# Optimization experiments

Measured on AMD Instinct MI355X. Metric: run time of the kernel, lower is better.

The kernel has to match this reference:

```python
import jax, jax.numpy as jnp
import numpy as np

B, IN, N, OUT = 65536, 512, 256, 64  # batch, in_size, neurons, out_size


def setup_inputs() -> dict:
    key = jax.random.key(0)
    k1, k2, k3, k4 = jax.random.split(key, 4)
    return {
        "x": jax.random.normal(k1, (B, IN), jnp.float32),
        "W_lin": jax.random.normal(k2, (IN, N + OUT), jnp.float32),   # nlinear
        "W_nl": jax.random.normal(k3, (N - 1, N), jnp.float32),        # padded nonlinear[i] rows
        "W_out": jax.random.normal(k4, (OUT, N), jnp.float32),         # output_weights[0:out_size]
    }


def reference(x, W_lin, W_nl, W_out):
    act = jnp.tanh
    lin = x @ W_lin  # [B, N+OUT]
    # row i of nonlinear weights is valid only for entries 0..i (length i+1)
    tri_mask = (jnp.arange(N)[None, :] <= jnp.arange(N - 1)[:, None]).astype(lin.dtype)
    Wm = W_nl * tri_mask  # [N-1, N]
    # growing accumulator, fixed-size buffer; position 0 = lin[0] + 1
    acc0 = jnp.zeros((x.shape[0], N), lin.dtype).at[:, 0].set(lin[:, 0] + 1.0)
    col = jnp.arange(N)[None, :]

    def step(acc, inp):
        w, l, i = inp  # w: [N] masked weights, l: [B] = lin[:, i], i: scalar step
        v = jnp.sum(act(acc) * w[None, :], axis=1) + l + 1.0  # [B]
        acc = jnp.where(col == (i + 1), v[:, None], acc)
        return acc, None

    xs = (Wm, lin[:, : N - 1].T, jnp.arange(N - 1))
    acc, _ = jax.lax.scan(step, acc0, xs)
    # outs[i] = act(t) @ output_weights[i] + lin[neurons + i] + 1
    out = act(acc) @ W_out.T + lin[:, N:] + 1.0  # [B, OUT]
    return out
```

## Files before the change

### kernel.cpp

```cpp
#include <hip/hip_runtime.h>
#include <hip/hip_bf16.h>

typedef _Float16 f16x8 __attribute__((ext_vector_type(8)));
typedef unsigned short u16x8 __attribute__((ext_vector_type(8)));
typedef float f32x4 __attribute__((ext_vector_type(4)));
typedef unsigned int u32x4 __attribute__((ext_vector_type(4)));

static __device__ __forceinline__ unsigned short h2u(_Float16 h) {
    return __builtin_bit_cast(unsigned short, h);
}
static __device__ __forceinline__ float fast_tanh(float x) {
    float e = __expf(2.0f * x);
    return 1.0f - 2.0f / (e + 1.0f);
}

__global__ void cascade_prep(const float* __restrict__ W_lin,
                             const float* __restrict__ W_nl,
                             const float* __restrict__ W_out,
                             unsigned short* __restrict__ wlin_h,
                             unsigned short* __restrict__ wlin_l,
                             unsigned short* __restrict__ wnl_h,
                             unsigned short* __restrict__ wnl_l,
                             unsigned short* __restrict__ wout_h,
                             unsigned short* __restrict__ wout_l,
                             float* __restrict__ wcol) {
    int idx = blockIdx.x * blockDim.x + threadIdx.x;
    int stride = gridDim.x * blockDim.x;
    for (int i = idx; i < 320 * 512; i += stride) {
        int n = i >> 9, k = i & 511;
        float w = W_lin[k * 320 + n];
        _Float16 h = (_Float16)w;
        wlin_h[i] = h2u(h);
        wlin_l[i] = h2u((_Float16)(w - (float)h));
    }
    for (int i = idx; i < 255 * 256; i += stride) {
        int r = i >> 8, k = i & 255;
        float w = (k <= r) ? W_nl[i] : 0.0f;
        _Float16 h = (_Float16)w;
        wnl_h[i] = h2u(h);
        wnl_l[i] = h2u((_Float16)(w - (float)h));
    }
    for (int i = idx; i < 64 * 256; i += stride) {
        float w = W_out[i];
        _Float16 h = (_Float16)w;
        wout_h[i] = h2u(h);
        wout_l[i] = h2u((_Float16)(w - (float)h));
    }
    for (int i = idx; i < 256; i += stride) {
        int b = i >> 5, u = i & 31;
        float* dst = wcol + b * 496 + (31 * u - (u * (u - 1)) / 2);
        for (int j = u + 1; j < 32; ++j)
            dst[j - u - 1] = W_nl[(size_t)(b * 32 + j - 1) * 256 + b * 32 + u];
    }
}

__global__ __launch_bounds__(512, 1) void lin_gemm(
    const float* __restrict__ x,
    const unsigned short* __restrict__ wlin_h,
    const unsigned short* __restrict__ wlin_l,
    float* __restrict__ linc,
    float* __restrict__ lino) {

    __shared__ _Float16 bufH[2][16 * 520];
    __shared__ _Float16 bufL[2][16 * 520];

    const int tid = threadIdx.x;
    const int wv  = tid >> 6;
    const int l15 = tid & 15;
    const int g   = (tid & 63) >> 4;
    const long row0 = (long)blockIdx.x * 128;

    f16x8 xfh[16], xfl[16];
    {
        const float* xp = x + (row0 + wv * 16 + l15) * 512 + g * 8;
        #pragma unroll
        for (int ks = 0; ks < 16; ++ks) {
            float4 p0 = *reinterpret_cast<const float4*>(xp + ks * 32);
            float4 p1 = *reinterpret_cast<const float4*>(xp + ks * 32 + 4);
            float av[8] = {p0.x, p0.y, p0.z, p0.w, p1.x, p1.y, p1.z, p1.w};
            f16x8 fh, fl;
            #pragma unroll
            for (int e = 0; e < 8; ++e) {
                _Float16 hh = (_Float16)av[e];
                fh[e] = hh;
                fl[e] = (_Float16)(av[e] - (float)hh);
            }
            xfh[ks] = fh;
            xfl[ks] = fl;
        }
    }

    u16x8 rh[2], rl[2];
    #define STAGE_LOAD(nt)                                                     \
        {                                                                      \
            _Pragma("unroll")                                                  \
            for (int it = 0; it < 2; ++it) {                                   \
                int flat = it * 4096 + tid * 8;                                \
                int r = flat >> 9, c = flat & 511;                             \
                rh[it] = *reinterpret_cast<const u16x8*>(                      \
                    wlin_h + (size_t)((nt) * 16 + r) * 512 + c);               \
                rl[it] = *reinterpret_cast<const u16x8*>(                      \
                    wlin_l + (size_t)((nt) * 16 + r) * 512 + c);               \
            }                                                                  \
        }
    #define STAGE_WRITE(buf)                                                   \
        {                                                                      \
            _Pragma("unroll")                                                  \
            for (int it = 0; it < 2; ++it) {                                   \
                int flat = it * 4096 + tid * 8;                                \
                int r = flat >> 9, c = flat & 511;                             \
                *reinterpret_cast<u16x8*>(&bufH[buf][r * 520 + c]) =           \
                    __builtin_bit_cast(u16x8, rh[it]);                         \
                *reinterpret_cast<u16x8*>(&bufL[buf][r * 520 + c]) =           \
                    __builtin_bit_cast(u16x8, rl[it]);                         \
            }                                                                  \
        }

    STAGE_LOAD(0);
    STAGE_WRITE(0);
    __syncthreads();

    int cur = 0;
    for (int nt = 0; nt < 20; ++nt) {
        if (nt < 19) STAGE_LOAD(nt + 1);

        f32x4 acc = (f32x4){0.f, 0.f, 0.f, 0.f};
        if (nt < 16) {
            #pragma unroll
            for (int ks = 0; ks < 16; ++ks) {
                f16x8 bh = *reinterpret_cast<const f16x8*>(
                    &bufH[cur][l15 * 520 + ks * 32 + g * 8]);
                f16x8 bl = *reinterpret_cast<const f16x8*>(
                    &bufL[cur][l15 * 520 + ks * 32 + g * 8]);
                acc = __builtin_amdgcn_mfma_f32_16x16x32_f16(xfh[ks], bh, acc, 0, 0, 0);
                acc = __builtin_amdgcn_mfma_f32_16x16x32_f16(xfl[ks], bh, acc, 0, 0, 0);
                acc = __builtin_amdgcn_mfma_f32_16x16x32_f16(xfh[ks], bl, acc, 0, 0, 0);
            }
            #pragma unroll
            for (int j = 0; j < 4; ++j)
                linc[(row0 + wv * 16 + g * 4 + j) * 256 + nt * 16 + l15] = acc[j];
        } else {
            #pragma unroll
            for (int ks = 0; ks < 16; ++ks) {
                f16x8 bh = *reinterpret_cast<const f16x8*>(
                    &bufH[cur][l15 * 520 + ks * 32 + g * 8]);
                acc = __builtin_amdgcn_mfma_f32_16x16x32_f16(xfh[ks], bh, acc, 0, 0, 0);
            }
            #pragma unroll
            for (int j = 0; j < 4; ++j)
                lino[(row0 + wv * 16 + g * 4 + j) * 64 + (nt - 16) * 16 + l15] = acc[j];
        }

        if (nt < 19) STAGE_WRITE(cur ^ 1);
        __syncthreads();
        cur ^= 1;
    }
    #undef STAGE_LOAD
    #undef STAGE_WRITE
}

static __device__ __forceinline__ void hist_frag(const unsigned int* hp,
                                                 f16x8* ah, f16x8* al) {
    u32x4 a0 = *reinterpret_cast<const u32x4*>(hp);
    u32x4 a1 = *reinterpret_cast<const u32x4*>(hp + 4);
    u32x4 hx, lx;
    hx[0] = (a0[0] & 0xffffu) | (a0[1] << 16);
    hx[1] = (a0[2] & 0xffffu) | (a0[3] << 16);
    hx[2] = (a1[0] & 0xffffu) | (a1[1] << 16);
    hx[3] = (a1[2] & 0xffffu) | (a1[3] << 16);
    lx[0] = (a0[0] >> 16) | (a0[1] & 0xffff0000u);
    lx[1] = (a0[2] >> 16) | (a0[3] & 0xffff0000u);
    lx[2] = (a1[0] >> 16) | (a1[1] & 0xffff0000u);
    lx[3] = (a1[2] >> 16) | (a1[3] & 0xffff0000u);
    *ah = __builtin_bit_cast(f16x8, hx);
    *al = __builtin_bit_cast(f16x8, lx);
}

__global__ __launch_bounds__(64, 2) void cascade_casc(
    float* linc,
    const float* __restrict__ lino,
    const float* __restrict__ wcol,
    const unsigned short* __restrict__ wnl_h,
    const unsigned short* __restrict__ wnl_l,
    const unsigned short* __restrict__ wout_h,
    const unsigned short* __restrict__ wout_l,
    float* __restrict__ out) {

    __shared__ float conT[32 * 36];
    __shared__ float linT[32 * 36];
    __shared__ float wslab[500];

    const int l   = threadIdx.x;
    const int l15 = l & 15;
    const int g   = l >> 4;
    const int r   = l & 31;
    const long row0 = (long)blockIdx.x * 32;

    unsigned int* histc = reinterpret_cast<unsigned int*>(linc);
    float carry = 0.0f;

    for (int b = 0; b < 8; ++b) {
        #pragma unroll
        for (int it = 0; it < 4; ++it) {
            int flat = it * 256 + l * 4;
            int rr = flat >> 5, c4 = flat & 31;
            float4 v = *reinterpret_cast<const float4*>(
                linc + (row0 + rr) * 256 + b * 32 + c4);
            *reinterpret_cast<float4*>(&linT[rr * 36 + c4]) = v;
        }
        {
            int i0 = l * 4;
            if (i0 < 496) {
                float4 v = *reinterpret_cast<const float4*>(wcol + b * 496 + i0);
                *reinterpret_cast<float4*>(&wslab[i0]) = v;
            }
            int i1 = 256 + l * 4;
            if (i1 < 496) {
                float4 v = *reinterpret_cast<const float4*>(wcol + b * 496 + i1);
                *reinterpret_cast<float4*>(&wslab[i1]) = v;
            }
        }

        f32x4 accC[2][2];
        #pragma unroll
        for (int m = 0; m < 2; ++m)
            #pragma unroll
            for (int n2 = 0; n2 < 2; ++n2)
                accC[m][n2] = (f32x4){0.f, 0.f, 0.f, 0.f};
        for (int kc = 0; kc < b; ++kc) {
            f16x8 ah[2], al[2];
            #pragma unroll
            for (int m = 0; m < 2; ++m)
                hist_frag(histc + (row0 + m * 16 + l15) * 256 + kc * 32 + g * 8,
                          &ah[m], &al[m]);
            #pragma unroll
            for (int n2 = 0; n2 < 2; ++n2) {
                const size_t wrow = (size_t)(b * 32 + n2 * 16 + l15 - 1) * 256 + kc * 32 + g * 8;
                f16x8 bh = __builtin_bit_cast(f16x8, *reinterpret_cast<const u16x8*>(wnl_h + wrow));
                f16x8 bl = __builtin_bit_cast(f16x8, *reinterpret_cast<const u16x8*>(wnl_l + wrow));
                #pragma unroll
                for (int m = 0; m < 2; ++m) {
                    accC[m][n2] = __builtin_amdgcn_mfma_f32_16x16x32_f16(ah[m], bh, accC[m][n2], 0, 0, 0);
                    accC[m][n2] = __builtin_amdgcn_mfma_f32_16x16x32_f16(al[m], bh, accC[m][n2], 0, 0, 0);
                    accC[m][n2] = __builtin_amdgcn_mfma_f32_16x16x32_f16(ah[m], bl, accC[m][n2], 0, 0, 0);
                }
            }
        }
        #pragma unroll
        for (int m = 0; m < 2; ++m)
            #pragma unroll
            for (int n2 = 0; n2 < 2; ++n2)
                #pragma unroll
                for (int j = 0; j < 4; ++j)
                    conT[(m * 16 + g * 4 + j) * 36 + n2 * 16 + l15] = accC[m][n2][j];
        __syncthreads();

        if (b == 0) carry = linT[r * 36];

        float acc[32];
        #pragma unroll
        for (int j = 0; j < 32; ++j) acc[j] = 0.0f;
        float lastlin = carry;
        #pragma unroll
        for (int u8 = 0; u8 < 4; ++u8) {
            float4 cw0 = *reinterpret_cast<const float4*>(&conT[r * 36 + u8 * 8]);
            float4 cw1 = *reinterpret_cast<const float4*>(&conT[r * 36 + u8 * 8 + 4]);
            float4 lw0 = *reinterpret_cast<const float4*>(&linT[r * 36 + u8 * 8]);
            float4 lw1 = *reinterpret_cast<const float4*>(&linT[r * 36 + u8 * 8 + 4]);
            float conw[8] = {cw0.x, cw0.y, cw0.z, cw0.w, cw1.x, cw1.y, cw1.z, cw1.w};
            float linw[8] = {lw0.x, lw0.y, lw0.z, lw0.w, lw1.x, lw1.y, lw1.z, lw1.w};
            unsigned int pk[8];
            #pragma unroll
            for (int v = 0; v < 8; ++v) {
                const int u = u8 * 8 + v;
                float lv = (v == 0) ? lastlin : linw[v - 1];
                float vv = acc[u] + conw[v] + lv + 1.0f;
                float tv = fast_tanh(vv);
                _Float16 hv = (_Float16)tv;
                _Float16 lo = (_Float16)(tv - (float)hv);
                pk[v] = (unsigned int)h2u(hv) | ((unsigned int)h2u(lo) << 16);
                const float* wu = wslab + (31 * u - (u * (u - 1)) / 2);
                #pragma unroll
                for (int j = u + 1; j < 32; ++j)
                    acc[j] = fmaf(tv, wu[j - u - 1], acc[j]);
            }
            lastlin = linw[7];
            if (l < 32) {
                long hb = (row0 + r) * 256 + b * 32 + u8 * 8;
                *reinterpret_cast<u32x4*>(histc + hb) = (u32x4){pk[0], pk[1], pk[2], pk[3]};
                *reinterpret_cast<u32x4*>(histc + hb + 4) = (u32x4){pk[4], pk[5], pk[6], pk[7]};
            }
        }
        carry = lastlin;
        __syncthreads();
    }

    #pragma unroll
    for (int m = 0; m < 2; ++m) {
        #pragma unroll
        for (int n = 0; n < 4; ++n) {
            f32x4 acc = (f32x4){0.f, 0.f, 0.f, 0.f};
            #pragma unroll
            for (int kc = 0; kc < 8; ++kc) {
                f16x8 ah, al;
                hist_frag(histc + (row0 + m * 16 + l15) * 256 + kc * 32 + g * 8, &ah, &al);
                const size_t wrow = (size_t)(n * 16 + l15) * 256 + kc * 32 + g * 8;
                f16x8 bh = __builtin_bit_cast(f16x8, *reinterpret_cast<const u16x8*>(wout_h + wrow));
                f16x8 bl = __builtin_bit_cast(f16x8, *reinterpret_cast<const u16x8*>(wout_l + wrow));
                acc = __builtin_amdgcn_mfma_f32_16x16x32_f16(ah, bh, acc, 0, 0, 0);
                acc = __builtin_amdgcn_mfma_f32_16x16x32_f16(al, bh, acc, 0, 0, 0);
                acc = __builtin_amdgcn_mfma_f32_16x16x32_f16(ah, bl, acc, 0, 0, 0);
            }
            #pragma unroll
            for (int j = 0; j < 4; ++j) {
                long rr = row0 + m * 16 + g * 4 + j;
                int c = n * 16 + l15;
                out[rr * 64 + c] = acc[j] + lino[rr * 64 + c] + 1.0f;
            }
        }
    }
}

extern "C" void kernel_launch(void* const* d_in, const int* in_sizes, int n_in,
                              void* d_out, int out_size, void* d_ws, size_t ws_size,
                              hipStream_t stream) {
    (void)in_sizes; (void)n_in; (void)out_size; (void)ws_size;
    const float* x     = (const float*)d_in[0];
    const float* W_lin = (const float*)d_in[1];
    const float* W_nl  = (const float*)d_in[2];
    const float* W_out = (const float*)d_in[3];
    float* out = (float*)d_out;

    char* ws = (char*)d_ws;
    unsigned short* wlin_h = (unsigned short*)(ws);
    unsigned short* wlin_l = (unsigned short*)(ws + 327680);
    unsigned short* wnl_h  = (unsigned short*)(ws + 916480);
    unsigned short* wnl_l  = (unsigned short*)(ws + 1047040);
    unsigned short* wout_h = (unsigned short*)(ws + 1177600);
    unsigned short* wout_l = (unsigned short*)(ws + 1210368);
    float*          wcol   = (float*)(ws + 1243136);
    float*          linc   = (float*)(ws + 1259008);
    float*          lino   = (float*)(ws + 68367872);

    cascade_prep<<<256, 256, 0, stream>>>(W_lin, W_nl, W_out,
                                          wlin_h, wlin_l, wnl_h, wnl_l,
                                          wout_h, wout_l, wcol);
    lin_gemm<<<512, 512, 0, stream>>>(x, wlin_h, wlin_l, linc, lino);
    cascade_casc<<<65536 / 32, 64, 0, stream>>>(linc, lino, wcol,
                                                wnl_h, wnl_l, wout_h, wout_l, out);
}
```

Before: 245.7 us.

## Keep cascade history in registers and remap block indices across XCDs

The cascade kernel no longer writes the packed tanh history back into the global linc buffer and re-reads it for every later block and for the output GEMM. Each 32-neuron block is staged through a small LDS buffer and then held in a fully unrolled register array, so global stores and reloads are removed. Both GEMM kernels also permute blockIdx so that consecutive row tiles land on the same XCD, which may improve L2 locality. The cost is a large register footprint (pf holds 8x2x2 u32x4 per lane) and full unrolling of the b loop, which could cause spills or lower occupancy.

```diff
diff --git a/kernel.cpp b/kernel.cpp
--- a/kernel.cpp
+++ b/kernel.cpp
@@ -68,7 +68,8 @@
     const int wv  = tid >> 6;
     const int l15 = tid & 15;
     const int g   = (tid & 63) >> 4;
-    const long row0 = (long)blockIdx.x * 128;
+    const int s = (blockIdx.x & 7) * 64 + (blockIdx.x >> 3);
+    const long row0 = (long)s * 128;
 
     f16x8 xfh[16], xfl[16];
     {
@@ -159,10 +160,8 @@
     #undef STAGE_WRITE
 }
 
-static __device__ __forceinline__ void hist_frag(const unsigned int* hp,
+static __device__ __forceinline__ void unpack_pf(u32x4 a0, u32x4 a1,
                                                  f16x8* ah, f16x8* al) {
-    u32x4 a0 = *reinterpret_cast<const u32x4*>(hp);
-    u32x4 a1 = *reinterpret_cast<const u32x4*>(hp + 4);
     u32x4 hx, lx;
     hx[0] = (a0[0] & 0xffffu) | (a0[1] << 16);
     hx[1] = (a0[2] & 0xffffu) | (a0[3] << 16);
@@ -177,7 +176,7 @@
 }
 
 __global__ __launch_bounds__(64, 2) void cascade_casc(
-    float* linc,
+    const float* __restrict__ linc,
     const float* __restrict__ lino,
     const float* __restrict__ wcol,
     const unsigned short* __restrict__ wnl_h,
@@ -189,16 +188,19 @@
     __shared__ float conT[32 * 36];
     __shared__ float linT[32 * 36];
     __shared__ float wslab[500];
+    __shared__ unsigned int lbuf[32 * 36];
 
     const int l   = threadIdx.x;
     const int l15 = l & 15;
     const int g   = l >> 4;
     const int r   = l & 31;
-    const long row0 = (long)blockIdx.x * 32;
-
-    unsigned int* histc = reinterpret_cast<unsigned int*>(linc);
+    const int s = (blockIdx.x & 7) * 256 + (blockIdx.x >> 3);
+    const long row0 = (long)s * 32;
+
+    u32x4 pf[8][2][2];
     float carry = 0.0f;
 
+    #pragma unroll
     for (int b = 0; b < 8; ++b) {
         #pragma unroll
         for (int it = 0; it < 4; ++it) {
@@ -227,22 +229,24 @@
             #pragma unroll
             for (int n2 = 0; n2 < 2; ++n2)
                 accC[m][n2] = (f32x4){0.f, 0.f, 0.f, 0.f};
-        for (int kc = 0; kc < b; ++kc) {
-            f16x8 ah[2], al[2];
-            #pragma unroll
-            for (int m = 0; m < 2; ++m)
-                hist_frag(histc + (row0 + m * 16 + l15) * 256 + kc * 32 + g * 8,
-                          &ah[m], &al[m]);
-            #pragma unroll
-            for (int n2 = 0; n2 < 2; ++n2) {
-                const size_t wrow = (size_t)(b * 32 + n2 * 16 + l15 - 1) * 256 + kc * 32 + g * 8;
-                f16x8 bh = __builtin_bit_cast(f16x8, *reinterpret_cast<const u16x8*>(wnl_h + wrow));
-                f16x8 bl = __builtin_bit_cast(f16x8, *reinterpret_cast<const u16x8*>(wnl_l + wrow));
+        #pragma unroll
+        for (int kc = 0; kc < 7; ++kc) {
+            if (kc < b) {
+                f16x8 ah[2], al[2];
                 #pragma unroll
-                for (int m = 0; m < 2; ++m) {
-                    accC[m][n2] = __builtin_amdgcn_mfma_f32_16x16x32_f16(ah[m], bh, accC[m][n2], 0, 0, 0);
-                    accC[m][n2] = __builtin_amdgcn_mfma_f32_16x16x32_f16(al[m], bh, accC[m][n2], 0, 0, 0);
-                    accC[m][n2] = __builtin_amdgcn_mfma_f32_16x16x32_f16(ah[m], bl, accC[m][n2], 0, 0, 0);
+                for (int m = 0; m < 2; ++m)
+                    unpack_pf(pf[kc][m][0], pf[kc][m][1], &ah[m], &al[m]);
+                #pragma unroll
+                for (int n2 = 0; n2 < 2; ++n2) {
+                    const size_t wrow = (size_t)(b * 32 + n2 * 16 + l15 - 1) * 256 + kc * 32 + g * 8;
+                    f16x8 bh = __builtin_bit_cast(f16x8, *reinterpret_cast<const u16x8*>(wnl_h + wrow));
+                    f16x8 bl = __builtin_bit_cast(f16x8, *reinterpret_cast<const u16x8*>(wnl_l + wrow));
+                    #pragma unroll
+                    for (int m = 0; m < 2; ++m) {
+                        accC[m][n2] = __builtin_amdgcn_mfma_f32_16x16x32_f16(ah[m], bh, accC[m][n2], 0, 0, 0);
+                        accC[m][n2] = __builtin_amdgcn_mfma_f32_16x16x32_f16(al[m], bh, accC[m][n2], 0, 0, 0);
+                        accC[m][n2] = __builtin_amdgcn_mfma_f32_16x16x32_f16(ah[m], bl, accC[m][n2], 0, 0, 0);
+                    }
                 }
             }
         }
@@ -286,13 +290,21 @@
             }
             lastlin = linw[7];
             if (l < 32) {
-                long hb = (row0 + r) * 256 + b * 32 + u8 * 8;
-                *reinterpret_cast<u32x4*>(histc + hb) = (u32x4){pk[0], pk[1], pk[2], pk[3]};
-                *reinterpret_cast<u32x4*>(histc + hb + 4) = (u32x4){pk[4], pk[5], pk[6], pk[7]};
+                *reinterpret_cast<u32x4*>(&lbuf[r * 36 + u8 * 8]) =
+                    (u32x4){pk[0], pk[1], pk[2], pk[3]};
+                *reinterpret_cast<u32x4*>(&lbuf[r * 36 + u8 * 8 + 4]) =
+                    (u32x4){pk[4], pk[5], pk[6], pk[7]};
             }
         }
         carry = lastlin;
         __syncthreads();
+
+        #pragma unroll
+        for (int m = 0; m < 2; ++m) {
+            const unsigned int* p = &lbuf[(l15 + 16 * m) * 36 + g * 8];
+            pf[b][m][0] = *reinterpret_cast<const u32x4*>(p);
+            pf[b][m][1] = *reinterpret_cast<const u32x4*>(p + 4);
+        }
     }
 
     #pragma unroll
@@ -303,7 +315,7 @@
             #pragma unroll
             for (int kc = 0; kc < 8; ++kc) {
                 f16x8 ah, al;
-                hist_frag(histc + (row0 + m * 16 + l15) * 256 + kc * 32 + g * 8, &ah, &al);
+                unpack_pf(pf[kc][m][0], pf[kc][m][1], &ah, &al);
                 const size_t wrow = (size_t)(n * 16 + l15) * 256 + kc * 32 + g * 8;
                 f16x8 bh = __builtin_bit_cast(f16x8, *reinterpret_cast<const u16x8*>(wout_h + wrow));
                 f16x8 bl = __builtin_bit_cast(f16x8, *reinterpret_cast<const u16x8*>(wout_l + wrow));
@@ -346,6 +358,6 @@
                                           wlin_h, wlin_l, wnl_h, wnl_l,
                                           wout_h, wout_l, wcol);
     lin_gemm<<<512, 512, 0, stream>>>(x, wlin_h, wlin_l, linc, lino);
-    cascade_casc<<<65536 / 32, 64, 0, stream>>>(linc, lino, wcol,
-                                                wnl_h, wnl_l, wout_h, wout_l, out);
-}
+    cascade_casc<<<2048, 64, 0, stream>>>(linc, lino, wcol,
+                                          wnl_h, wnl_l, wout_h, wout_l, out);
+}
```

Result: slower. 300.4 us (+22.3%).
